# Kernel tuning notes

Hardware: AMD Instinct MI355X
Metric: run time of the kernel (lower is better)

Reference implementation:

```python
import jax, jax.numpy as jnp
import numpy as np

N = 20000      # nodes (spots)
D = 256        # embed_dim
H = 4          # n_heads
DH = D // H    # head dim
L = 2          # n_layers
E = 320000     # edges (avg degree 16)
K = 48         # static padded-neighbor cap (>= true max degree for this data)
EPS = 1e-5
NEG = -1e30


def setup_inputs() -> dict:
    key = jax.random.key(0)
    ks = jax.random.split(key, 8)
    s = 0.05
    return {
        "expr_embed": jax.random.normal(ks[0], (N, D), jnp.float32),
        "spatial_embed": jax.random.normal(ks[1], (N, D), jnp.float32),
        "in_proj_w": jax.random.normal(ks[2], (L, 3 * D, D), jnp.float32) * s,
        "in_proj_b": jnp.zeros((L, 3 * D), jnp.float32),
        "out_proj_w": jax.random.normal(ks[3], (L, D, D), jnp.float32) * s,
        "out_proj_b": jnp.zeros((L, D), jnp.float32),
        "ffn_w1": jax.random.normal(ks[4], (L, 2 * D, D), jnp.float32) * s,
        "ffn_b1": jnp.zeros((L, 2 * D), jnp.float32),
        "ffn_w2": jax.random.normal(ks[5], (L, D, 2 * D), jnp.float32) * s,
        "ffn_b2": jnp.zeros((L, D), jnp.float32),
        "ln1_g": jnp.ones((L, D), jnp.float32),
        "ln1_b": jnp.zeros((L, D), jnp.float32),
        "ln2_g": jnp.ones((L, D), jnp.float32),
        "ln2_b": jnp.zeros((L, D), jnp.float32),
        "edge_index": jax.random.randint(ks[6], (2, E), 0, N, jnp.int32),
    }


def _build_neighbors(edge_index):
    """Padded neighbor indices (N,K) and key_padding_mask (N,K) (True = pad)."""
    src, tgt = edge_index[0], edge_index[1]
    counts = jnp.zeros((N,), jnp.int32).at[tgt].add(1)
    order = jnp.argsort(tgt)                       # group edges by target
    src_s, tgt_s = src[order], tgt[order]
    offsets = jnp.concatenate([jnp.zeros((1,), jnp.int32),
                               jnp.cumsum(counts)[:-1].astype(jnp.int32)])
    pos = jnp.arange(E, dtype=jnp.int32) - offsets[tgt_s]
    pos = jnp.where(pos < K, pos, K)               # K is out-of-bounds -> dropped
    nbr = jnp.zeros((N, K), jnp.int32).at[tgt_s, pos].set(src_s, mode='drop')
    pad = jnp.ones((N, K), bool).at[tgt_s, pos].set(False, mode='drop')
    iso = counts == 0                              # isolated spots attend to self
    nbr = nbr.at[:, 0].set(jnp.where(iso, jnp.arange(N, dtype=jnp.int32), nbr[:, 0]))
    pad = pad.at[:, 0].set(jnp.where(iso, False, pad[:, 0]))
    return nbr, pad


def _layernorm(x, g, b):
    mu = jnp.mean(x, -1, keepdims=True)
    var = jnp.var(x, -1, keepdims=True)
    return (x - mu) * jax.lax.rsqrt(var + EPS) * g + b


def _forward(expr_embed, spatial_embed, in_proj_w, in_proj_b, out_proj_w,
             out_proj_b, ffn_w1, ffn_b1, ffn_w2, ffn_b2,
             ln1_g, ln1_b, ln2_g, ln2_b, nbr, pad):
    x = expr_embed
    scale = 1.0 / jnp.sqrt(jnp.asarray(DH, x.dtype))
    for i in range(L):
        Wq, Wk, Wv = jnp.split(in_proj_w[i], 3, axis=0)
        bq, bk, bv = jnp.split(in_proj_b[i], 3, axis=0)
        q = (x @ Wq.T + bq).reshape(N, H, DH)
        # project spatial once, gather projected rows (same math as gather-then-project)
        k = (spatial_embed @ Wk.T + bk)[nbr].reshape(N, K, H, DH)
        v = (spatial_embed @ Wv.T + bv)[nbr].reshape(N, K, H, DH)
        scores = jnp.einsum('nhd,nkhd->nhk', q, k) * scale      # (N,H,K)
        scores = jnp.where(pad[:, None, :], NEG, scores)
        attn = jax.nn.softmax(scores, axis=-1)
        ao = jnp.einsum('nhk,nkhd->nhd', attn, v).reshape(N, D)
        ao = ao @ out_proj_w[i].T + out_proj_b[i]
        x = _layernorm(x + ao, ln1_g[i], ln1_b[i])
        h = jax.nn.gelu(x @ ffn_w1[i].T + ffn_b1[i], approximate=False)
        h = h @ ffn_w2[i].T + ffn_b2[i]
        x = _layernorm(x + h, ln2_g[i], ln2_b[i])
    return x


def reference(expr_embed, spatial_embed, in_proj_w, in_proj_b, out_proj_w,
              out_proj_b, ffn_w1, ffn_b1, ffn_w2, ffn_b2,
              ln1_g, ln1_b, ln2_g, ln2_b, edge_index):
    nbr, pad = _build_neighbors(edge_index.astype(jnp.int32))
    return _forward(expr_embed, spatial_embed, in_proj_w, in_proj_b, out_proj_w,
                    out_proj_b, ffn_w1, ffn_b1, ffn_w2, ffn_b2,
                    ln1_g, ln1_b, ln2_g, ln2_b, nbr, pad)
```

## Files before the change

kernel.cpp:

```cpp
#include <hip/hip_runtime.h>

#define N_NODES 20000
#define DIM 256
#define NHEAD 4
#define DHEAD 64
#define NLAYER 2
#define NEDGE 320000
#define KCAP 48
#define NBM64 313
#define NBM128 157

typedef __bf16 v8bf __attribute__((ext_vector_type(8)));
typedef __bf16 v2bf __attribute__((ext_vector_type(2)));
typedef float v4f __attribute__((ext_vector_type(4)));

union U32 { unsigned u; v2bf v; };

__device__ __forceinline__ unsigned short f2bf(float f) {
    unsigned u = __float_as_uint(f);
    unsigned r = u + 0x7FFFu + ((u >> 16) & 1u);
    return (unsigned short)(r >> 16);
}
__device__ __forceinline__ float bflo(unsigned u) { return __uint_as_float(u << 16); }
__device__ __forceinline__ float bfhi(unsigned u) { return __uint_as_float(u & 0xFFFF0000u); }

__device__ __forceinline__ void gl2lds(const void* g, void* l) {
    __builtin_amdgcn_global_load_lds(
        (const __attribute__((address_space(1))) unsigned int*)g,
        (__attribute__((address_space(3))) unsigned int*)l, 16, 0, 0);
}

__device__ __forceinline__ void stage8(const unsigned short* __restrict__ g0,
                                       size_t stride_e, unsigned short* lds) {
    const int l = threadIdx.x & 63;
    const int r = l >> 3;
    const int c = (l & 7) ^ r;
    gl2lds(g0 + (size_t)r * stride_e + c * 8, lds);
}
__device__ __forceinline__ void stage8c(const unsigned short* __restrict__ base,
                                        int row0, int rowmax, size_t stride_e,
                                        int k0, unsigned short* lds) {
    const int l = threadIdx.x & 63;
    const int r = l >> 3;
    const int c = (l & 7) ^ r;
    int row = row0 + r; row = row > rowmax ? rowmax : row;
    gl2lds(base + (size_t)row * stride_e + k0 + c * 8, lds);
}

__device__ __forceinline__ v8bf frag_read(const unsigned short* lds, int row, int col2) {
    const int bo = row * 128 + (col2 ^ ((row & 7) << 4));
    return *(const v8bf*)((const char*)lds + bo);
}

__global__ void sniffzero_kernel(const unsigned short* __restrict__ p,
                                 int* __restrict__ flag, int* __restrict__ cnt) {
    if (blockIdx.x == 0) {
        __shared__ int s;
        if (threadIdx.x == 0) s = 0;
        __syncthreads();
        int c = 0;
        for (int i = threadIdx.x; i < 4096; i += 256) {
            unsigned short u = p[i];
            unsigned e = (u >> 7) & 0xFFu;
            if (e == 0xFFu) c++;
            else if (e == 0u && (u & 0x7Fu)) c++;
        }
        atomicAdd(&s, c);
        __syncthreads();
        if (threadIdx.x == 0) flag[0] = (s >= 4) ? 1 : 0;
    } else {
        int i = (blockIdx.x - 1) * 256 + threadIdx.x;
        if (i < N_NODES) cnt[i] = 0;
    }
}

struct ConvBfArgs { const void* src[6]; unsigned short* dst[6]; int n[6]; };

__global__ void conv_bf16_kernel(ConvBfArgs a, const int* __restrict__ flag) {
    const int t  = blockIdx.y;
    const int n  = a.n[t];
    const int i0 = (blockIdx.x * 256 + threadIdx.x) * 4;
    if (i0 >= n) return;
    unsigned short* dst = a.dst[t];
    if (flag[0]) {
        float4 v = *(const float4*)((const float*)a.src[t] + i0);
        ushort4 o;
        o.x = f2bf(v.x); o.y = f2bf(v.y); o.z = f2bf(v.z); o.w = f2bf(v.w);
        *(ushort4*)(dst + i0) = o;
    } else {
        ushort4 u = *(const ushort4*)((const unsigned short*)a.src[t] + i0);
        *(ushort4*)(dst + i0) = u;
    }
}

struct ConvF32Args { const void* src[8]; float* dst[8]; int n[8]; };

__global__ void conv_f32_kernel(ConvF32Args a, const int* __restrict__ flag) {
    const int t  = blockIdx.y;
    const int n  = a.n[t];
    const int i0 = (blockIdx.x * 256 + threadIdx.x) * 4;
    if (i0 >= n) return;
    float* dst = a.dst[t];
    if (flag[0]) {
        float4 v = *(const float4*)((const float*)a.src[t] + i0);
        *(float4*)(dst + i0) = v;
    } else {
        ushort4 u = *(const ushort4*)((const unsigned short*)a.src[t] + i0);
        *(float4*)(dst + i0) = make_float4(bflo(u.x), bflo(u.y), bflo(u.z), bflo(u.w));
    }
}

__global__ void build_nbr_kernel(const int* __restrict__ ei,
                                 int* __restrict__ cnt, int* __restrict__ nbr) {
    int e = blockIdx.x * 256 + threadIdx.x;
    if (e >= NEDGE) return;
    int s = ei[e];
    int t = ei[NEDGE + e];
    int slot = atomicAdd(&cnt[t], 1);
    if (slot < KCAP) nbr[t * KCAP + slot] = s;
}

__device__ __forceinline__ void gemm_body128(
    unsigned short* At, unsigned short* Bt,
    const unsigned short* __restrict__ A, const unsigned short* __restrict__ B,
    const float* __restrict__ bias, unsigned short* __restrict__ C,
    int M, int Nc, int Kd, int m0, int nB, int nC, int do_gelu)
{
    const int tid  = threadIdx.x;
    const int wave = tid >> 6;
    const int lane = tid & 63;
    const int wr   = (wave >> 1) * 64;
    const int wc   = (wave & 1) * 64;
    const int lm   = lane & 15;
    const int lk   = (lane >> 4) * 8;

    v4f acc[4][4] = {};

    for (int k0 = 0; k0 < Kd; k0 += 64) {
#pragma unroll
        for (int g2 = 0; g2 < 4; ++g2) {
            const int rr = wave * 32 + g2 * 8;
            stage8c(A, m0 + rr, M - 1, Kd, k0, At + rr * 64);
            stage8(B + (size_t)(nB + rr) * Kd + k0, Kd, Bt + rr * 64);
        }
        __syncthreads();

#pragma unroll
        for (int ks = 0; ks < 2; ++ks) {
            v8bf af[4], bq[4];
#pragma unroll
            for (int mi = 0; mi < 4; ++mi)
                af[mi] = frag_read(At, wr + mi * 16 + lm, (ks * 32 + lk) * 2);
#pragma unroll
            for (int ni = 0; ni < 4; ++ni)
                bq[ni] = frag_read(Bt, wc + ni * 16 + lm, (ks * 32 + lk) * 2);
#pragma unroll
            for (int mi = 0; mi < 4; ++mi)
#pragma unroll
                for (int ni = 0; ni < 4; ++ni)
                    acc[mi][ni] = __builtin_amdgcn_mfma_f32_16x16x32_bf16(
                        af[mi], bq[ni], acc[mi][ni], 0, 0, 0);
        }
        __syncthreads();
    }

    const int rq = (lane >> 4) << 2;
#pragma unroll
    for (int ni = 0; ni < 4; ++ni) {
        int colb = wc + ni * 16 + lm;
        float bv = bias[nB + colb];
        int colc = nC + colb;
#pragma unroll
        for (int mi = 0; mi < 4; ++mi) {
#pragma unroll
            for (int r = 0; r < 4; ++r) {
                int row = m0 + wr + mi * 16 + rq + r;
                if (row >= M) continue;
                float v = acc[mi][ni][r] + bv;
                if (do_gelu) v = 0.5f * v * (1.0f + erff(v * 0.7071067811865475f));
                C[(size_t)row * Nc + colc] = f2bf(v);
            }
        }
    }
}

__global__ __launch_bounds__(256, 3) void gemm_kernel(
    const unsigned short* __restrict__ A, const unsigned short* __restrict__ B,
    const float* __restrict__ bias, unsigned short* __restrict__ C,
    int M, int Nc, int Kd, int do_gelu)
{
    __shared__ __align__(1024) unsigned short At[128 * 64];
    __shared__ __align__(1024) unsigned short Bt[128 * 64];
    const int n0 = blockIdx.y * 128;
    gemm_body128(At, Bt, A, B, bias, C, M, Nc, Kd, blockIdx.x * 128, n0, n0, do_gelu);
}

__global__ __launch_bounds__(256, 3) void qkv_kernel(
    const unsigned short* __restrict__ x, const unsigned short* __restrict__ spat,
    const unsigned short* __restrict__ W, const float* __restrict__ bias,
    unsigned short* __restrict__ q, unsigned short* __restrict__ kv, int M)
{
    __shared__ __align__(1024) unsigned short At[128 * 64];
    __shared__ __align__(1024) unsigned short Bt[128 * 64];
    const int y = blockIdx.y;
    const unsigned short* A = (y < 2) ? x : spat;
    unsigned short*       C = (y < 2) ? q : kv;
    const int Nc = (y < 2) ? 256 : 512;
    const int nB = y * 128;
    const int nC = (y < 2) ? nB : nB - 256;
    gemm_body128(At, Bt, A, W, bias, C, M, Nc, 256, blockIdx.x * 128, nB, nC, 0);
}

__global__ __launch_bounds__(256) void gemm_ln_kernel(
    const unsigned short* __restrict__ A, const unsigned short* __restrict__ B,
    const float* __restrict__ bias, const unsigned short* __restrict__ xres,
    const float* __restrict__ g, const float* __restrict__ bb,
    unsigned short* __restrict__ xout, void* __restrict__ dout,
    int M, int Kd, int final_out, const int* __restrict__ flag)
{
    __shared__ __align__(1024) unsigned short At[64 * 64];
    __shared__ __align__(1024) unsigned short Bt[256 * 64];
    __shared__ float partS[4][64], partSS[4][64];
    __shared__ float totMu[64], totR[64];

    const int tid  = threadIdx.x;
    const int m0   = blockIdx.x * 64;
    const int wave = tid >> 6;
    const int lane = tid & 63;
    const int wn0  = wave * 64;
    const int lm   = lane & 15;
    const int lk   = (lane >> 4) * 8;

    v4f acc[4][4] = {};

    for (int k0 = 0; k0 < Kd; k0 += 64) {
#pragma unroll
        for (int g2 = 0; g2 < 2; ++g2) {
            const int rr = wave * 16 + g2 * 8;
            stage8c(A, m0 + rr, M - 1, Kd, k0, At + rr * 64);
        }
#pragma unroll
        for (int g2 = 0; g2 < 8; ++g2) {
            const int rr = wave * 64 + g2 * 8;
            stage8(B + (size_t)rr * Kd + k0, Kd, Bt + rr * 64);
        }
        __syncthreads();

#pragma unroll
        for (int ks = 0; ks < 2; ++ks) {
            v8bf af[4], bq[4];
#pragma unroll
            for (int mi = 0; mi < 4; ++mi)
                af[mi] = frag_read(At, mi * 16 + lm, (ks * 32 + lk) * 2);
#pragma unroll
            for (int ni = 0; ni < 4; ++ni)
                bq[ni] = frag_read(Bt, wn0 + ni * 16 + lm, (ks * 32 + lk) * 2);
#pragma unroll
            for (int mi = 0; mi < 4; ++mi)
#pragma unroll
                for (int ni = 0; ni < 4; ++ni)
                    acc[mi][ni] = __builtin_amdgcn_mfma_f32_16x16x32_bf16(
                        af[mi], bq[ni], acc[mi][ni], 0, 0, 0);
        }
        __syncthreads();
    }

    const int rq = (lane >> 4) << 2;
    float gv[4], bv2[4], biasv[4];
#pragma unroll
    for (int ni = 0; ni < 4; ++ni) {
        int col = wn0 + ni * 16 + lm;
        biasv[ni] = bias[col];
        gv[ni]    = g[col];
        bv2[ni]   = bb[col];
    }

    float sl[4][4] = {}, ssl[4][4] = {};
#pragma unroll
    for (int mi = 0; mi < 4; ++mi) {
#pragma unroll
        for (int r = 0; r < 4; ++r) {
            int row = m0 + mi * 16 + rq + r;
#pragma unroll
            for (int ni = 0; ni < 4; ++ni) {
                int col = wn0 + ni * 16 + lm;
                float resv = bflo((unsigned)xres[(size_t)row * DIM + col]);
                float v = acc[mi][ni][r] + biasv[ni] + resv;
                acc[mi][ni][r] = v;
                sl[mi][r]  += v;
                ssl[mi][r] += v * v;
            }
        }
    }
#pragma unroll
    for (int mi = 0; mi < 4; ++mi)
#pragma unroll
        for (int r = 0; r < 4; ++r) {
#pragma unroll
            for (int m = 1; m <= 8; m <<= 1) {
                sl[mi][r]  += __shfl_xor(sl[mi][r],  m, 64);
                ssl[mi][r] += __shfl_xor(ssl[mi][r], m, 64);
            }
        }
    if (lm == 0) {
#pragma unroll
        for (int mi = 0; mi < 4; ++mi)
#pragma unroll
            for (int r = 0; r < 4; ++r) {
                partS[wave][mi * 16 + rq + r]  = sl[mi][r];
                partSS[wave][mi * 16 + rq + r] = ssl[mi][r];
            }
    }
    __syncthreads();
    if (tid < 64) {
        float S = partS[0][tid] + partS[1][tid] + partS[2][tid] + partS[3][tid];
        float SS = partSS[0][tid] + partSS[1][tid] + partSS[2][tid] + partSS[3][tid];
        float mu  = S * (1.0f / DIM);
        float var = SS * (1.0f / DIM) - mu * mu;
        totMu[tid] = mu;
        totR[tid]  = rsqrtf(var + 1e-5f);
    }
    __syncthreads();

#pragma unroll
    for (int mi = 0; mi < 4; ++mi) {
#pragma unroll
        for (int r = 0; r < 4; ++r) {
            int lrow = mi * 16 + rq + r;
            int row  = m0 + lrow;
            if (row >= M) continue;
            float mu = totMu[lrow];
            float rv = totR[lrow];
#pragma unroll
            for (int ni = 0; ni < 4; ++ni) {
                int col = wn0 + ni * 16 + lm;
                float o = (acc[mi][ni][r] - mu) * rv * gv[ni] + bv2[ni];
                if (final_out) {
                    if (flag[0]) ((float*)dout)[(size_t)row * DIM + col] = o;
                    else ((unsigned short*)dout)[(size_t)row * DIM + col] = f2bf(o);
                } else {
                    xout[(size_t)row * DIM + col] = f2bf(o);
                }
            }
        }
    }
}

__global__ __launch_bounds__(256) void attn_kernel(
    const unsigned short* __restrict__ q,
    const unsigned short* __restrict__ kv,
    const int* __restrict__ nbr,
    const int* __restrict__ cnt,
    unsigned short* __restrict__ ao)
{
    const int n    = blockIdx.x;
    const int tid  = threadIdx.x;
    const int h    = tid >> 6;
    const int lane = tid & 63;

    __shared__ float sc[NHEAD][KCAP];
    __shared__ int   nbs[NHEAD][KCAP];

    int deg = cnt[n];
    if (deg > KCAP) deg = KCAP;
    const bool iso = (deg == 0);
    if (iso) deg = 1;

    if (lane < KCAP)
        nbs[h][lane] = (lane < deg) ? (iso ? n : nbr[n * KCAP + lane]) : 0;

    const int sub = lane & 7;
    const int grp = lane >> 3;
    const uint4 qu = *(const uint4*)&q[(size_t)n * DIM + h * DHEAD + sub * 8];
    const unsigned short* kbase = kv + h * DHEAD + sub * 8;
    const int nit = (deg + 7) >> 3;

    const int quarter = lane >> 4;
    const int d0      = (lane & 15) * 4;
    const unsigned short* vbase = kv + 256 + h * DHEAD + d0;
    const int dmax = (deg + 3) & ~3;
    const int npv  = dmax >> 2;

    uint4 ku[6];
#pragma unroll
    for (int it = 0; it < 6; ++it) {
        if (it < nit) {
            int nb = nbs[h][it * 8 + grp];
            ku[it] = *(const uint4*)&kbase[(size_t)nb * 512];
        }
    }
    uint2 vu[8];
#pragma unroll
    for (int it = 0; it < 8; ++it) {
        if (it < npv) {
            int nb = nbs[h][it * 4 + quarter];
            vu[it] = *(const uint2*)&vbase[(size_t)nb * 512];
        }
    }

#pragma unroll
    for (int it = 0; it < 6; ++it) {
        if (it < nit) {
            int j = it * 8 + grp;
            uint4 kz = ku[it];
#if __has_builtin(__builtin_amdgcn_fdot2_f32_bf16)
            U32 a0{qu.x}, a1{qu.y}, a2{qu.z}, a3{qu.w};
            U32 b0{kz.x}, b1{kz.y}, b2{kz.z}, b3{kz.w};
            float p = __builtin_amdgcn_fdot2_f32_bf16(a0.v, b0.v, 0.0f, false);
            p = __builtin_amdgcn_fdot2_f32_bf16(a1.v, b1.v, p, false);
            p = __builtin_amdgcn_fdot2_f32_bf16(a2.v, b2.v, p, false);
            p = __builtin_amdgcn_fdot2_f32_bf16(a3.v, b3.v, p, false);
#else
            float p = bflo(qu.x) * bflo(kz.x);
            p = fmaf(bfhi(qu.x), bfhi(kz.x), p);
            p = fmaf(bflo(qu.y), bflo(kz.y), p);
            p = fmaf(bfhi(qu.y), bfhi(kz.y), p);
            p = fmaf(bflo(qu.z), bflo(kz.z), p);
            p = fmaf(bfhi(qu.z), bfhi(kz.z), p);
            p = fmaf(bflo(qu.w), bflo(kz.w), p);
            p = fmaf(bfhi(qu.w), bfhi(kz.w), p);
#endif
            p += __shfl_xor(p, 1, 64);
            p += __shfl_xor(p, 2, 64);
            p += __shfl_xor(p, 4, 64);
            if (sub == 0 && j < deg) sc[h][j] = p * 0.125f;
        }
    }

    {
        float s  = (lane < deg) ? sc[h][lane] : -1e30f;
        float mx = s;
#pragma unroll
        for (int m = 32; m >= 1; m >>= 1) mx = fmaxf(mx, __shfl_xor(mx, m, 64));
        float e   = (lane < deg) ? __expf(s - mx) : 0.0f;
        float sum = e;
#pragma unroll
        for (int m = 32; m >= 1; m >>= 1) sum += __shfl_xor(sum, m, 64);
        float inv = 1.0f / sum;
        if (lane < KCAP) sc[h][lane] = e * inv;
    }

    {
        float a0 = 0.f, a1 = 0.f, a2 = 0.f, a3 = 0.f;
#pragma unroll
        for (int it = 0; it < 8; ++it) {
            if (it < npv) {
                float w = sc[h][it * 4 + quarter];
                uint2 u = vu[it];
                a0 = fmaf(w, bflo(u.x), a0);
                a1 = fmaf(w, bfhi(u.x), a1);
                a2 = fmaf(w, bflo(u.y), a2);
                a3 = fmaf(w, bfhi(u.y), a3);
            }
        }
        for (int j = 32; j < dmax; j += 4) {
            int j0 = j + quarter;
            int nb = nbs[h][j0];
            uint2 u = *(const uint2*)&vbase[(size_t)nb * 512];
            float w = sc[h][j0];
            a0 = fmaf(w, bflo(u.x), a0);
            a1 = fmaf(w, bfhi(u.x), a1);
            a2 = fmaf(w, bflo(u.y), a2);
            a3 = fmaf(w, bfhi(u.y), a3);
        }
        a0 += __shfl_xor(a0, 16, 64); a0 += __shfl_xor(a0, 32, 64);
        a1 += __shfl_xor(a1, 16, 64); a1 += __shfl_xor(a1, 32, 64);
        a2 += __shfl_xor(a2, 16, 64); a2 += __shfl_xor(a2, 32, 64);
        a3 += __shfl_xor(a3, 16, 64); a3 += __shfl_xor(a3, 32, 64);
        if (lane < 16) {
            uint2 o;
            o.x = (unsigned)f2bf(a0) | ((unsigned)f2bf(a1) << 16);
            o.y = (unsigned)f2bf(a2) | ((unsigned)f2bf(a3) << 16);
            *(uint2*)&ao[(size_t)n * DIM + h * DHEAD + d0] = o;
        }
    }
}

extern "C" void kernel_launch(void* const* d_in, const int* in_sizes, int n_in,
                              void* d_out, int out_size, void* d_ws, size_t ws_size,
                              hipStream_t stream) {
    const int* ei = (const int*)d_in[14];

    char* ws = (char*)d_ws;
    size_t off = 0;
    auto alloc = [&](size_t bytes) -> void* {
        void* p = ws + off;
        off = (off + bytes + 255) & ~(size_t)255;
        return p;
    };

    const int bidx[6] = { 0, 1, 2, 4, 6, 8 };
    const int bnn[6]  = { N_NODES * DIM, N_NODES * DIM,
                          NLAYER * 3 * DIM * DIM, NLAYER * DIM * DIM,
                          NLAYER * 2 * DIM * DIM, NLAYER * DIM * 2 * DIM };
    ConvBfArgs cb;
    unsigned short* canb[6];
    for (int i = 0; i < 6; ++i) {
        canb[i] = (unsigned short*)alloc((size_t)bnn[i] * 2);
        cb.src[i] = d_in[bidx[i]];
        cb.dst[i] = canb[i];
        cb.n[i]   = bnn[i];
    }
    const unsigned short* expr_b = canb[0];
    const unsigned short* spat_b = canb[1];
    const unsigned short* ipw    = canb[2];
    const unsigned short* opw    = canb[3];
    const unsigned short* w1     = canb[4];
    const unsigned short* w2     = canb[5];

    const int fidx[8] = { 3, 5, 7, 9, 10, 11, 12, 13 };
    const int fn[8]   = { NLAYER * 3 * DIM, NLAYER * DIM, NLAYER * 2 * DIM,
                          NLAYER * DIM, NLAYER * DIM, NLAYER * DIM,
                          NLAYER * DIM, NLAYER * DIM };
    ConvF32Args cf;
    float* canf[8];
    for (int i = 0; i < 8; ++i) {
        canf[i] = (float*)alloc((size_t)fn[i] * 4);
        cf.src[i] = d_in[fidx[i]];
        cf.dst[i] = canf[i];
        cf.n[i]   = fn[i];
    }

    unsigned short* x_buf  = (unsigned short*)alloc((size_t)N_NODES * DIM * 2);
    unsigned short* q_buf  = (unsigned short*)alloc((size_t)N_NODES * DIM * 2);
    unsigned short* kv_buf = (unsigned short*)alloc((size_t)N_NODES * 2 * DIM * 2);
    unsigned short* ao_buf = (unsigned short*)alloc((size_t)N_NODES * DIM * 2);
    unsigned short* h_buf  = (unsigned short*)alloc((size_t)N_NODES * 2 * DIM * 2);
    int* cnt  = (int*)alloc((size_t)N_NODES * 4);
    int* nbr  = (int*)alloc((size_t)N_NODES * KCAP * 4);
    int* flag = (int*)alloc(256);

    sniffzero_kernel<<<1 + (N_NODES + 255) / 256, 256, 0, stream>>>(
        (const unsigned short*)d_in[0], flag, cnt);
    conv_bf16_kernel<<<dim3((N_NODES * DIM) / 1024, 6), 256, 0, stream>>>(cb, flag);
    conv_f32_kernel<<<dim3(2, 8), 256, 0, stream>>>(cf, flag);
    build_nbr_kernel<<<(NEDGE + 255) / 256, 256, 0, stream>>>(ei, cnt, nbr);

    for (int i = 0; i < NLAYER; ++i) {
        const unsigned short* Wqkv = ipw + (size_t)i * 3 * DIM * DIM;
        const float*          bqkv = canf[0] + (size_t)i * 3 * DIM;
        const unsigned short* xin  = (i == 0) ? expr_b : x_buf;

        qkv_kernel<<<dim3(NBM128, 6), 256, 0, stream>>>(
            xin, spat_b, Wqkv, bqkv, q_buf, kv_buf, N_NODES);
        attn_kernel<<<N_NODES, 256, 0, stream>>>(q_buf, kv_buf, nbr, cnt, ao_buf);
        gemm_ln_kernel<<<NBM64, 256, 0, stream>>>(
            ao_buf, opw + (size_t)i * DIM * DIM, canf[1] + (size_t)i * DIM,
            xin, canf[4] + (size_t)i * DIM, canf[5] + (size_t)i * DIM,
            x_buf, nullptr, N_NODES, DIM, 0, flag);
        gemm_kernel<<<dim3(NBM128, 4), 256, 0, stream>>>(
            x_buf, w1 + (size_t)i * 2 * DIM * DIM, canf[2] + (size_t)i * 2 * DIM,
            h_buf, N_NODES, 2 * DIM, DIM, 1);
        gemm_ln_kernel<<<NBM64, 256, 0, stream>>>(
            h_buf, w2 + (size_t)i * DIM * 2 * DIM, canf[3] + (size_t)i * DIM,
            x_buf, canf[6] + (size_t)i * DIM, canf[7] + (size_t)i * DIM,
            x_buf, d_out, N_NODES, 2 * DIM, (i == NLAYER - 1) ? 1 : 0, flag);
    }
}
```

Baseline: 418.9 us.

## Double-buffer GEMM LDS tiles with K=32 steps and new swizzle

```diff
diff --git a/kernel.cpp b/kernel.cpp
--- a/kernel.cpp
+++ b/kernel.cpp
@@ -30,25 +30,25 @@
         (__attribute__((address_space(3))) unsigned int*)l, 16, 0, 0);
 }
 
-__device__ __forceinline__ void stage8(const unsigned short* __restrict__ g0,
-                                       size_t stride_e, unsigned short* lds) {
+__device__ __forceinline__ void stage16(const unsigned short* __restrict__ g0,
+                                        size_t stride_e, unsigned short* lds) {
     const int l = threadIdx.x & 63;
-    const int r = l >> 3;
-    const int c = (l & 7) ^ r;
+    const int r = l >> 2;
+    const int c = (l & 3) ^ ((r >> 1) & 3);
     gl2lds(g0 + (size_t)r * stride_e + c * 8, lds);
 }
-__device__ __forceinline__ void stage8c(const unsigned short* __restrict__ base,
-                                        int row0, int rowmax, size_t stride_e,
-                                        int k0, unsigned short* lds) {
+__device__ __forceinline__ void stage16c(const unsigned short* __restrict__ base,
+                                         int row0, int rowmax, size_t stride_e,
+                                         int k0, unsigned short* lds) {
     const int l = threadIdx.x & 63;
-    const int r = l >> 3;
-    const int c = (l & 7) ^ r;
+    const int r = l >> 2;
+    const int c = (l & 3) ^ ((r >> 1) & 3);
     int row = row0 + r; row = row > rowmax ? rowmax : row;
     gl2lds(base + (size_t)row * stride_e + k0 + c * 8, lds);
 }
 
-__device__ __forceinline__ v8bf frag_read(const unsigned short* lds, int row, int col2) {
-    const int bo = row * 128 + (col2 ^ ((row & 7) << 4));
+__device__ __forceinline__ v8bf frag32(const unsigned short* lds, int row, int t) {
+    const int bo = row * 64 + (((t ^ ((row >> 1) & 3))) << 4);
     return *(const v8bf*)((const char*)lds + bo);
 }
 
@@ -132,35 +132,40 @@
     const int wr   = (wave >> 1) * 64;
     const int wc   = (wave & 1) * 64;
     const int lm   = lane & 15;
-    const int lk   = (lane >> 4) * 8;
+    const int lt   = lane >> 4;
 
     v4f acc[4][4] = {};
 
-    for (int k0 = 0; k0 < Kd; k0 += 64) {
-#pragma unroll
-        for (int g2 = 0; g2 < 4; ++g2) {
-            const int rr = wave * 32 + g2 * 8;
-            stage8c(A, m0 + rr, M - 1, Kd, k0, At + rr * 64);
-            stage8(B + (size_t)(nB + rr) * Kd + k0, Kd, Bt + rr * 64);
-        }
-        __syncthreads();
-
-#pragma unroll
-        for (int ks = 0; ks < 2; ++ks) {
-            v8bf af[4], bq[4];
-#pragma unroll
-            for (int mi = 0; mi < 4; ++mi)
-                af[mi] = frag_read(At, wr + mi * 16 + lm, (ks * 32 + lk) * 2);
+    const int r0 = wave * 32;
+    auto STAGE = [&](int buf, int k0) {
+        unsigned short* A_l = At + buf * (128 * 32);
+        unsigned short* B_l = Bt + buf * (128 * 32);
+        stage16c(A, m0 + r0,      M - 1, Kd, k0, A_l + r0 * 32);
+        stage16c(A, m0 + r0 + 16, M - 1, Kd, k0, A_l + (r0 + 16) * 32);
+        stage16(B + (size_t)(nB + r0) * Kd + k0,      Kd, B_l + r0 * 32);
+        stage16(B + (size_t)(nB + r0 + 16) * Kd + k0, Kd, B_l + (r0 + 16) * 32);
+    };
+
+    const int nt = Kd >> 5;
+    STAGE(0, 0);
+    __syncthreads();
+    for (int t = 0; t < nt; ++t) {
+        if (t + 1 < nt) STAGE((t + 1) & 1, (t + 1) * 32);
+        const unsigned short* A_l = At + (t & 1) * (128 * 32);
+        const unsigned short* B_l = Bt + (t & 1) * (128 * 32);
+        v8bf af[4], bq[4];
+#pragma unroll
+        for (int mi = 0; mi < 4; ++mi)
+            af[mi] = frag32(A_l, wr + mi * 16 + lm, lt);
+#pragma unroll
+        for (int ni = 0; ni < 4; ++ni)
+            bq[ni] = frag32(B_l, wc + ni * 16 + lm, lt);
+#pragma unroll
+        for (int mi = 0; mi < 4; ++mi)
 #pragma unroll
             for (int ni = 0; ni < 4; ++ni)
-                bq[ni] = frag_read(Bt, wc + ni * 16 + lm, (ks * 32 + lk) * 2);
-#pragma unroll
-            for (int mi = 0; mi < 4; ++mi)
-#pragma unroll
-                for (int ni = 0; ni < 4; ++ni)
-                    acc[mi][ni] = __builtin_amdgcn_mfma_f32_16x16x32_bf16(
-                        af[mi], bq[ni], acc[mi][ni], 0, 0, 0);
-        }
+                acc[mi][ni] = __builtin_amdgcn_mfma_f32_16x16x32_bf16(
+                    af[mi], bq[ni], acc[mi][ni], 0, 0, 0);
         __syncthreads();
     }
 
@@ -189,8 +194,8 @@
     const float* __restrict__ bias, unsigned short* __restrict__ C,
     int M, int Nc, int Kd, int do_gelu)
 {
-    __shared__ __align__(1024) unsigned short At[128 * 64];
-    __shared__ __align__(1024) unsigned short Bt[128 * 64];
+    __shared__ __align__(1024) unsigned short At[2 * 128 * 32];
+    __shared__ __align__(1024) unsigned short Bt[2 * 128 * 32];
     const int n0 = blockIdx.y * 128;
     gemm_body128(At, Bt, A, B, bias, C, M, Nc, Kd, blockIdx.x * 128, n0, n0, do_gelu);
 }
@@ -200,8 +205,8 @@
     const unsigned short* __restrict__ W, const float* __restrict__ bias,
     unsigned short* __restrict__ q, unsigned short* __restrict__ kv, int M)
 {
-    __shared__ __align__(1024) unsigned short At[128 * 64];
-    __shared__ __align__(1024) unsigned short Bt[128 * 64];
+    __shared__ __align__(1024) unsigned short At[2 * 128 * 32];
+    __shared__ __align__(1024) unsigned short Bt[2 * 128 * 32];
     const int y = blockIdx.y;
     const unsigned short* A = (y < 2) ? x : spat;
     unsigned short*       C = (y < 2) ? q : kv;
@@ -218,8 +223,8 @@
     unsigned short* __restrict__ xout, void* __restrict__ dout,
     int M, int Kd, int final_out, const int* __restrict__ flag)
 {
-    __shared__ __align__(1024) unsigned short At[64 * 64];
-    __shared__ __align__(1024) unsigned short Bt[256 * 64];
+    __shared__ __align__(1024) unsigned short At[2 * 64 * 32];
+    __shared__ __align__(1024) unsigned short Bt[2 * 256 * 32];
     __shared__ float partS[4][64], partSS[4][64];
     __shared__ float totMu[64], totR[64];
 
@@ -229,39 +234,41 @@
     const int lane = tid & 63;
     const int wn0  = wave * 64;
     const int lm   = lane & 15;
-    const int lk   = (lane >> 4) * 8;
+    const int lt   = lane >> 4;
 
     v4f acc[4][4] = {};
 
-    for (int k0 = 0; k0 < Kd; k0 += 64) {
-#pragma unroll
-        for (int g2 = 0; g2 < 2; ++g2) {
-            const int rr = wave * 16 + g2 * 8;
-            stage8c(A, m0 + rr, M - 1, Kd, k0, At + rr * 64);
-        }
-#pragma unroll
-        for (int g2 = 0; g2 < 8; ++g2) {
-            const int rr = wave * 64 + g2 * 8;
-            stage8(B + (size_t)rr * Kd + k0, Kd, Bt + rr * 64);
-        }
-        __syncthreads();
-
-#pragma unroll
-        for (int ks = 0; ks < 2; ++ks) {
-            v8bf af[4], bq[4];
-#pragma unroll
-            for (int mi = 0; mi < 4; ++mi)
-                af[mi] = frag_read(At, mi * 16 + lm, (ks * 32 + lk) * 2);
+    auto STAGE = [&](int buf, int k0) {
+        unsigned short* A_l = At + buf * (64 * 32);
+        unsigned short* B_l = Bt + buf * (256 * 32);
+        stage16c(A, m0 + wave * 16, M - 1, Kd, k0, A_l + wave * 16 * 32);
+#pragma unroll
+        for (int i = 0; i < 4; ++i) {
+            const int rr = wave * 64 + i * 16;
+            stage16(B + (size_t)rr * Kd + k0, Kd, B_l + rr * 32);
+        }
+    };
+
+    const int nt = Kd >> 5;
+    STAGE(0, 0);
+    __syncthreads();
+    for (int t = 0; t < nt; ++t) {
+        if (t + 1 < nt) STAGE((t + 1) & 1, (t + 1) * 32);
+        const unsigned short* A_l = At + (t & 1) * (64 * 32);
+        const unsigned short* B_l = Bt + (t & 1) * (256 * 32);
+        v8bf af[4], bq[4];
+#pragma unroll
+        for (int mi = 0; mi < 4; ++mi)
+            af[mi] = frag32(A_l, mi * 16 + lm, lt);
+#pragma unroll
+        for (int ni = 0; ni < 4; ++ni)
+            bq[ni] = frag32(B_l, wn0 + ni * 16 + lm, lt);
+#pragma unroll
+        for (int mi = 0; mi < 4; ++mi)
 #pragma unroll
             for (int ni = 0; ni < 4; ++ni)
-                bq[ni] = frag_read(Bt, wn0 + ni * 16 + lm, (ks * 32 + lk) * 2);
-#pragma unroll
-            for (int mi = 0; mi < 4; ++mi)
-#pragma unroll
-                for (int ni = 0; ni < 4; ++ni)
-                    acc[mi][ni] = __builtin_amdgcn_mfma_f32_16x16x32_bf16(
-                        af[mi], bq[ni], acc[mi][ni], 0, 0, 0);
-        }
+                acc[mi][ni] = __builtin_amdgcn_mfma_f32_16x16x32_bf16(
+                    af[mi], bq[ni], acc[mi][ni], 0, 0, 0);
         __syncthreads();
     }
 
@@ -397,6 +404,7 @@
             vu[it] = *(const uint2*)&vbase[(size_t)nb * 512];
         }
     }
+    __builtin_amdgcn_sched_barrier(0);
 
 #pragma unroll
     for (int it = 0; it < 6; ++it) {
```

Result: slower. 430.7 us (+2.8%).
